# Kernel tuning notes

Hardware: AMD Instinct MI355X
Metric: run time of the kernel (lower is better)

The kernel has to match this reference:

```python
import jax, jax.numpy as jnp
from jax import lax
import numpy as np

K = 2000      # self.k: entries kept per sample
T_SC = 3      # number of IHT iterations
DN = ('NCHW', 'OIHW', 'NCHW')


def keep_k_largest(X, k):
    # Per-sample hard threshold: keep the k largest-magnitude entries of the
    # flattened [C,H,W] activations, zero the rest (exactly k kept, as in argsort).
    B = X.shape[0]
    flat = X.reshape(B, -1)                                # [B, N]
    _, idx = lax.top_k(jnp.abs(flat), k)                   # [B, k]
    vals = jnp.take_along_axis(flat, idx, axis=1)          # [B, k]
    out = jnp.zeros_like(flat).at[jnp.arange(B)[:, None], idx].set(vals)
    return out.reshape(X.shape)


def _D_apply(X, W_D):
    # ConvTranspose2d(numb_atom -> dp_channels), stride 1, no padding:
    # full correlation with the spatially flipped, io-swapped kernel.
    kh, kw = W_D.shape[2], W_D.shape[3]
    Wt = jnp.flip(jnp.transpose(W_D, (1, 0, 2, 3)), (2, 3))  # [dp, atoms, kh, kw]
    return lax.conv_general_dilated(X, Wt, (1, 1),
                                    [(kh - 1, kh - 1), (kw - 1, kw - 1)],
                                    dimension_numbers=DN)


def _Dt_apply(Z, W_D):
    # Conv2d(dp_channels -> numb_atom) VALID; D_trans.weight = D.weight.permute(0,1,3,2)
    Wt = jnp.transpose(W_D, (0, 1, 3, 2))                  # [atoms, dp, kh, kw]
    return lax.conv_general_dilated(Z, Wt, (1, 1), 'VALID', dimension_numbers=DN)


def setup_inputs() -> dict:
    key = jax.random.key(0)
    k1, k2, k3 = jax.random.split(key, 3)
    Y = jax.random.normal(k1, (32, 3, 64, 64), jnp.float32)
    X0 = jax.random.normal(k2, (32, 128, 57, 57), jnp.float32)   # random init X in forward
    W_D = jax.random.normal(k3, (128, 3, 8, 8), jnp.float32) * 0.05
    return {"Y": Y, "X0": X0, "W_D": W_D}


def reference(Y, X0, W_D):
    # HT_arg = X - D_trans(D(X) - Y); then T_SC hard-threshold iterations.
    HT_arg = X0 - _Dt_apply(_D_apply(X0, W_D) - Y, W_D)
    X = HT_arg
    for i in range(T_SC):
        X = keep_k_largest(HT_arg, K)
        if i < T_SC - 1:  # final HT_arg update in the original is unused
            HT_arg = X - _Dt_apply(_D_apply(X, W_D) - Y, W_D)
    return X
```

## Files before the change

kernel.cpp:

```cpp
#include <hip/hip_runtime.h>

#define BATCH 32
#define ATOMS 128
#define CCH 3
#define XH 57
#define XW 57
#define OHH 64
#define OWW 64
#define KSEL 2000
#define PIX (XH*XW)
#define NPS (ATOMS*PIX)
#define NTOT (BATCH*NPS)
#define RPS (CCH*OHH*OWW)
#define RTOT (BATCH*RPS)
#define CANDCAP 32768
#define NW 24576
#define WSEG 102
#define ZWORDS (32*2048 + 32*1024)

__global__ __launch_bounds__(256) void prep_k(const float* __restrict__ Wg,
    double* __restrict__ WDd, double* __restrict__ Wt2d,
    const float* __restrict__ Y, double* __restrict__ Rd,
    unsigned* __restrict__ zbuf) {
  int e = blockIdx.x * 256 + threadIdx.x;
  if (e < NW) {
    {
      int kw = e & 7; int t = e >> 3; int c = t % 3; t /= 3; int kh = t & 7; int a = t >> 3;
      WDd[e] = (double)Wg[(a*3 + c)*64 + kh*8 + kw];
    }
    {
      int a = e & 127; int t = e >> 7; int j = t & 7; int i = (t >> 3) & 7; int c = t >> 6;
      Wt2d[e] = (double)Wg[(a*3 + c)*64 + j*8 + i];
    }
  }
  if (e < RTOT) Rd[e] = -(double)Y[e];
  if (e < ZWORDS + 64) zbuf[e] = 0;
}

__global__ __launch_bounds__(256) void convD_k(const float* __restrict__ X,
    const double* __restrict__ WDd, double* __restrict__ Rd) {
  __shared__ double Xs[4][11][72];
  int p = blockIdx.x;
  int lg = (p & 7) * 256 + (p >> 3);
  int b = lg >> 6; int rem = lg & 63;
  int band = rem >> 2, quarter = rem & 3;
  int row0 = band * 4;
  int a_base = quarter * 32;
  int tid = threadIdx.x;
  int ox = tid & 63;
  int wv = __builtin_amdgcn_readfirstlane(tid >> 6);
  const float* Xb = X + (size_t)b * NPS;

  double acc[4][3];
#pragma unroll
  for (int ty = 0; ty < 4; ++ty)
#pragma unroll
    for (int c = 0; c < 3; ++c) acc[ty][c] = 0.0;

  for (int ch = 0; ch < 8; ++ch) {
    __syncthreads();
    for (int e = tid; e < 4 * 11 * 72; e += 256) {
      int ai = e / 792; int rem2 = e - ai * 792;
      int r = rem2 / 72; int ss = rem2 - r * 72;
      int gy = row0 - 7 + r;
      int xcol = ss - 7;
      int a = a_base + ch * 4 + ai;
      float v = 0.0f;
      if ((unsigned)xcol < (unsigned)XW && (unsigned)gy < (unsigned)XH)
        v = Xb[a * PIX + gy * XW + xcol];
      Xs[ai][r][ss] = (double)v;
    }
    __syncthreads();
    {
      int a = a_base + ch * 4 + wv;
      const double* Wa = WDd + a * 192;
#pragma unroll
      for (int r = 0; r < 11; ++r) {
        int gy = row0 - 7 + r;
        if ((unsigned)gy >= (unsigned)XH) continue;
        double xd[8];
#pragma unroll
        for (int t = 0; t < 8; ++t) xd[t] = Xs[wv][r][ox + t];
#pragma unroll
        for (int ty = 0; ty < 4; ++ty) {
          int kh = ty + 7 - r;
          if ((unsigned)kh < 8u) {
            const double* Wk = Wa + kh * 24;
#pragma unroll
            for (int kw = 0; kw < 8; ++kw) {
              acc[ty][0] = fma(xd[7 - kw], Wk[kw],      acc[ty][0]);
              acc[ty][1] = fma(xd[7 - kw], Wk[8 + kw],  acc[ty][1]);
              acc[ty][2] = fma(xd[7 - kw], Wk[16 + kw], acc[ty][2]);
            }
          }
        }
      }
    }
  }
#pragma unroll
  for (int ty = 0; ty < 4; ++ty) {
    int oy = row0 + ty;
#pragma unroll
    for (int c = 0; c < 3; ++c)
      atomicAdd(&Rd[((size_t)(b * CCH + c) << 12) + (oy << 6) + ox], acc[ty][c]);
  }
}

__global__ __launch_bounds__(256) void convD_sparse_k(const float* __restrict__ Wg,
    const int* __restrict__ nzidx, const float* __restrict__ nzval,
    const float* __restrict__ Y, float* __restrict__ R) {
  __shared__ double accd[512];
  __shared__ float Wf[8192];
  __shared__ int   li[KSEL];
  __shared__ float lv[KSEL];
  int p = blockIdx.x;
  int lg = (p & 7) * 96 + (p >> 3);
  int s = lg / 24; int r = lg % 24; int c = r >> 3; int band = r & 7;
  int row0 = band * 8;
  int tid = threadIdx.x;
  for (int e = tid; e < 512; e += 256) accd[e] = 0.0;
  for (int e = tid; e < 8192; e += 256) {
    int a = e >> 6, k2 = e & 63;
    Wf[e] = Wg[(a * 3 + c) * 64 + k2];
  }
  for (int e = tid; e < KSEL; e += 256) {
    li[e] = nzidx[s * KSEL + e];
    lv[e] = nzval[s * KSEL + e];
  }
  __syncthreads();
  int slot = tid >> 3, kw = tid & 7;
  for (int e = slot; e < KSEL; e += 32) {
    int idx = li[e];
    int a = (int)((unsigned)idx / 3249u);
    int pp = idx - a * 3249;
    int y = (int)((unsigned)pp / 57u);
    int x = pp - y * 57;
    int dy = y - row0;
    if (dy < -7 || dy > 7) continue;
    double val = (double)lv[e];
    const float* wp = Wf + (a << 6) + kw;
#pragma unroll
    for (int kh = 0; kh < 8; ++kh) {
      int rr = dy + kh;
      if ((unsigned)rr < 8u)
        __hip_atomic_fetch_add(&accd[(rr << 6) + x + kw],
                               val * (double)wp[kh << 3],
                               __ATOMIC_RELAXED, __HIP_MEMORY_SCOPE_WORKGROUP);
    }
  }
  __syncthreads();
  const float* Yb = Y + (((size_t)(s * CCH + c)) << 12) + (row0 << 6);
  float* Rb = R + (((size_t)(s * CCH + c)) << 12) + (row0 << 6);
  for (int e = tid; e < 512; e += 256)
    Rb[e] = (float)(accd[e] - (double)Yb[e]);
}

template <typename TR>
__global__ __launch_bounds__(256) void convDt_k(const TR* __restrict__ R,
    const double* __restrict__ Wt2d, const float* __restrict__ Xprev,
    float* __restrict__ HT, unsigned* __restrict__ g1) {
  __shared__ float Rl[3][15][72];
  __shared__ unsigned hh[1024];
  int p = blockIdx.x;
  int lg = (p & 7) * 512 + (p >> 3);
  int b = lg >> 7; int rem = lg & 127; int ag = rem >> 3; int by = rem & 7;
  int row0 = by * 8;
  int a0 = ag * 8;
  int tid = threadIdx.x;
  for (int e = tid; e < 1024; e += 256) hh[e] = 0;
  for (int e = tid; e < 3 * 15 * 72; e += 256) {
    int c = e / (15 * 72); int r2 = e - c * (15 * 72);
    int rr = r2 / 72; int cc = r2 - rr * 72;
    int gr = row0 + rr;
    float v = 0.0f;
    if (cc < OWW && gr < OHH)
      v = (float)R[((size_t)(b * CCH + c) << 12) + (gr << 6) + cc];
    Rl[c][rr][cc] = v;
  }
  __syncthreads();
  int x = tid & 63, yg = tid >> 6;
  int yb = yg * 2;
  double acc[8][2];
#pragma unroll
  for (int aa = 0; aa < 8; ++aa) { acc[aa][0] = 0.0; acc[aa][1] = 0.0; }

#pragma unroll 1
  for (int c = 0; c < 3; ++c) {
#pragma unroll 1
    for (int j = 0; j < 8; ++j) {
      double rw[9];
#pragma unroll
      for (int r = 0; r < 9; ++r) rw[r] = (double)Rl[c][yb + r][x + j];
#pragma unroll
      for (int i = 0; i < 8; ++i) {
        const double* wp = Wt2d + ((c * 8 + i) * 8 + j) * 128 + a0;
#pragma unroll
        for (int aa = 0; aa < 8; ++aa) {
          double w = wp[aa];
          acc[aa][0] = fma(rw[i + 0], w, acc[aa][0]);
          acc[aa][1] = fma(rw[i + 1], w, acc[aa][1]);
        }
      }
    }
  }
  if (x < XW) {
#pragma unroll
    for (int ty = 0; ty < 2; ++ty) {
      int yy = row0 + yb + ty;
      if (yy < XH) {
#pragma unroll
        for (int aa = 0; aa < 8; ++aa) {
          size_t xo = (size_t)(b * ATOMS + a0 + aa) * PIX + yy * XW + x;
          float fv = (float)((double)Xprev[xo] - acc[aa][ty]);
          HT[xo] = fv;
          unsigned u = __float_as_uint(fv) & 0x7fffffffu;
          unsigned bin = u >> 20;
          atomicAdd(&hh[bin >> 1], 1u << ((bin & 1) << 4));
        }
      }
    }
  }
  __syncthreads();
  unsigned* gp = g1 + (size_t)b * 2048;
  for (int e = tid; e < 1024; e += 256) {
    unsigned v = hh[e];
    unsigned lo = v & 0xffffu, hi = v >> 16;
    if (lo) atomicAdd(&gp[2 * e], lo);
    if (hi) atomicAdd(&gp[2 * e + 1], hi);
  }
}

__global__ __launch_bounds__(256) void hist2_k(const float* __restrict__ HT,
    const unsigned* __restrict__ g1, unsigned* __restrict__ g2,
    int* __restrict__ cand, int* __restrict__ candcnt) {
  __shared__ unsigned h[1024];
  __shared__ unsigned part[256];
  __shared__ int lidx[4096];
  __shared__ int lcnt, lbase, b1_sh;
  int tid = threadIdx.x;
  int s = blockIdx.x >> 5;
  int chunk = blockIdx.x & 31;
  const unsigned* hg1 = g1 + (size_t)s * 2048;
  unsigned psum = 0;
#pragma unroll
  for (int e = 0; e < 8; ++e) psum += hg1[tid * 8 + e];
  part[tid] = psum;
  for (int e = tid; e < 1024; e += 256) h[e] = 0;
  if (tid == 0) lcnt = 0;
  __syncthreads();
  if (tid == 0) {
    int Kv = KSEL;
    unsigned cumBefore = 0;
    int bsel = 0;
    for (int q = 255; q >= 0; --q) {
      unsigned ps = part[q];
      if ((int)(cumBefore + ps) >= Kv) {
        for (int e = q * 8 + 7;; --e) {
          unsigned c2 = cumBefore + hg1[e];
          if ((int)c2 >= Kv) { bsel = e; break; }
          cumBefore = c2;
        }
        break;
      }
      cumBefore += ps;
    }
    b1_sh = bsel;
  }
  __syncthreads();
  unsigned pre = (unsigned)b1_sh;
  const uint4* U4 = (const uint4*)(HT + (size_t)s * NPS);
  for (int i4 = chunk * 256 + tid; i4 < NPS / 4; i4 += 32 * 256) {
    uint4 v = U4[i4];
    unsigned uu[4] = {v.x, v.y, v.z, v.w};
#pragma unroll
    for (int t = 0; t < 4; ++t) {
      unsigned u = uu[t] & 0x7fffffffu;
      if ((u >> 20) == pre) {
        atomicAdd(&h[(u >> 10) & 1023], 1u);
        int pos = atomicAdd(&lcnt, 1);
        if (pos < 4096) lidx[pos] = i4 * 4 + t;
      }
    }
  }
  __syncthreads();
  if (tid == 0) {
    int n = lcnt < 4096 ? lcnt : 4096;
    lbase = atomicAdd(&candcnt[s], n);
  }
  __syncthreads();
  int n = lcnt < 4096 ? lcnt : 4096;
  int base = lbase;
  for (int e = tid; e < n; e += 256) {
    int g = base + e;
    if (g < CANDCAP) cand[s * CANDCAP + g] = lidx[e];
  }
  for (int e = tid; e < 1024; e += 256)
    if (h[e]) atomicAdd(&g2[s * 1024 + e], h[e]);
}

__global__ __launch_bounds__(256) void pass3_k(const float* __restrict__ HT,
    const int* __restrict__ cand, int* __restrict__ candcnt,
    const unsigned* __restrict__ g1, const unsigned* __restrict__ g2,
    int* __restrict__ nzcnt, unsigned* __restrict__ tau_out,
    int* __restrict__ cutoff_out) {
  int s = blockIdx.x;
  __shared__ unsigned h[1024];
  __shared__ unsigned part[256];
  __shared__ int eqidx[1024];
  __shared__ int eqn;
  __shared__ unsigned tau_sh;
  __shared__ int k3_sh;
  __shared__ int b1_sh, k1_sh, b2_sh, k2_sh;
  int t = threadIdx.x;
  const unsigned* hg1 = g1 + (size_t)s * 2048;
  unsigned s1 = 0;
#pragma unroll
  for (int e = 0; e < 8; ++e) s1 += hg1[t * 8 + e];
  part[t] = s1;
  for (int e = t; e < 1024; e += 256) h[e] = 0;
  if (t == 0) eqn = 0;
  __syncthreads();
  if (t == 0) {
    int Kv = KSEL;
    unsigned cumBefore = 0;
    int bsel = 0;
    for (int q = 255; q >= 0; --q) {
      unsigned ps = part[q];
      if ((int)(cumBefore + ps) >= Kv) {
        for (int e = q * 8 + 7;; --e) {
          unsigned c2 = cumBefore + hg1[e];
          if ((int)c2 >= Kv) { bsel = e; break; }
          cumBefore = c2;
        }
        break;
      }
      cumBefore += ps;
    }
    b1_sh = bsel;
    k1_sh = Kv - (int)cumBefore;
  }
  __syncthreads();
  const unsigned* hg = g2 + s * 1024;
  unsigned s2 = 0;
#pragma unroll
  for (int e = 0; e < 4; ++e) s2 += hg[t * 4 + e];
  part[t] = s2;
  __syncthreads();
  if (t == 0) {
    int Kv = k1_sh;
    unsigned cumBefore = 0;
    int bsel = 0;
    for (int q = 255; q >= 0; --q) {
      unsigned ps = part[q];
      if ((int)(cumBefore + ps) >= Kv) {
        for (int e = q * 4 + 3;; --e) {
          unsigned c2 = cumBefore + hg[e];
          if ((int)c2 >= Kv) { bsel = e; break; }
          cumBefore = c2;
        }
        break;
      }
      cumBefore += ps;
    }
    b2_sh = bsel;
    k2_sh = Kv - (int)cumBefore;
  }
  __syncthreads();
  int n = candcnt[s];
  if (n > CANDCAP) n = CANDCAP;
  unsigned pre21 = (((unsigned)b1_sh) << 10) | (unsigned)b2_sh;
  const unsigned* U = (const unsigned*)(HT + (size_t)s * NPS);
  for (int e = t; e < n; e += 256) {
    int i = cand[s * CANDCAP + e];
    unsigned u = U[i] & 0x7fffffffu;
    if ((u >> 10) == pre21) atomicAdd(&h[u & 1023], 1u);
  }
  __syncthreads();
  if (t == 0) {
    int Kv = k2_sh;
    unsigned cumBefore = 0;
    int b3 = 0;
    for (int e = 1023; e >= 0; --e) {
      unsigned c2 = cumBefore + h[e];
      if ((int)c2 >= Kv) { b3 = e; break; }
      cumBefore = c2;
    }
    tau_sh = (pre21 << 10) | (unsigned)b3;
    k3_sh = Kv - (int)cumBefore;
  }
  __syncthreads();
  unsigned tau = tau_sh;
  for (int e = t; e < n; e += 256) {
    int i = cand[s * CANDCAP + e];
    unsigned u = U[i] & 0x7fffffffu;
    if (u == tau) {
      int pos = atomicAdd(&eqn, 1);
      if (pos < 1024) eqidx[pos] = i;
    }
  }
  __syncthreads();
  if (t == 0) {
    int m = eqn < 1024 ? eqn : 1024;
    int k3 = k3_sh;
    int cutoff;
    if (k3 >= m) {
      cutoff = 0x7fffffff;
    } else {
      int last = -1;
      for (int r = 0; r < k3; ++r) {
        int mn = 0x7fffffff;
        for (int q = 0; q < m; ++q) {
          int v = eqidx[q];
          if (v > last && v < mn) mn = v;
        }
        last = mn;
      }
      cutoff = last;
    }
    tau_out[s] = tau;
    cutoff_out[s] = cutoff;
    candcnt[s] = 0;
    nzcnt[s] = 0;
  }
}

__global__ __launch_bounds__(256) void write_k(const float* __restrict__ HT,
    const unsigned* __restrict__ tau, const int* __restrict__ cutoff,
    float* __restrict__ Xo, int* __restrict__ nzidx, float* __restrict__ nzval,
    int* __restrict__ nzcnt, unsigned* __restrict__ zbuf) {
  __shared__ int lidx[2048];
  __shared__ float lval[2048];
  __shared__ int lcnt, lbase;
  int s = blockIdx.x / WSEG;
  int seg = blockIdx.x % WSEG;
  int tid = threadIdx.x;
  bool emit = (nzidx != nullptr);
  if (zbuf) {
    int e = blockIdx.x * 256 + tid;
    if (e < ZWORDS) zbuf[e] = 0;
  }
  if (tid == 0) lcnt = 0;
  __syncthreads();
  unsigned tt = tau[s];
  int co = cutoff[s];
  size_t sbase = (size_t)s * NPS;
  const float4* H4 = (const float4*)(HT + sbase);
  float4* X4 = (float4*)(Xo + sbase);
  int f0 = seg * 1024;
#pragma unroll
  for (int rr = 0; rr < 4; ++rr) {
    int i4 = f0 + rr * 256 + tid;
    if (i4 < NPS / 4) {
      float4 v = H4[i4];
      float vv[4] = {v.x, v.y, v.z, v.w};
      float oo[4];
#pragma unroll
      for (int t = 0; t < 4; ++t) {
        int il = i4 * 4 + t;
        unsigned u = __float_as_uint(vv[t]) & 0x7fffffffu;
        bool keep = (u > tt) || (u == tt && il <= co);
        oo[t] = keep ? vv[t] : 0.0f;
        if (keep && emit) {
          int pos = atomicAdd(&lcnt, 1);
          if (pos < 2048) { lidx[pos] = il; lval[pos] = vv[t]; }
        }
      }
      X4[i4] = make_float4(oo[0], oo[1], oo[2], oo[3]);
    }
  }
  if (!emit) return;
  __syncthreads();
  if (tid == 0) lbase = atomicAdd(&nzcnt[s], lcnt);
  __syncthreads();
  int n = lcnt < 2048 ? lcnt : 2048;
  int base = lbase;
  for (int e = tid; e < n; e += 256) {
    int g = base + e;
    if (g < KSEL) { nzidx[s * KSEL + g] = lidx[e]; nzval[s * KSEL + g] = lval[e]; }
  }
}

extern "C" void kernel_launch(void* const* d_in, const int* in_sizes, int n_in,
                              void* d_out, int out_size, void* d_ws, size_t ws_size,
                              hipStream_t stream) {
  const float* Y  = (const float*)d_in[0];
  const float* X0 = (const float*)d_in[1];
  const float* Wg = (const float*)d_in[2];
  float* Xout = (float*)d_out;

  double* WDd  = (double*)d_ws;
  double* Wt2d = WDd + NW;
  float* HT   = (float*)(Wt2d + NW);
  float* Rbuf = HT + NTOT;
  double* Rd  = (double*)(Rbuf + RTOT);
  unsigned* g1 = (unsigned*)(Rd + RTOT);
  unsigned* g2 = g1 + 32 * 2048;
  int* candcnt = (int*)(g2 + 32 * 1024);
  int* nzcnt = candcnt + 32;
  unsigned* tau = (unsigned*)(nzcnt + 32);
  int* cutoff = (int*)(tau + 32);
  int* cand = cutoff + 32;
  int* nzidx = cand + 32 * CANDCAP;
  float* nzval = (float*)(nzidx + 32 * KSEL);

  prep_k<<<dim3((RTOT + 255) / 256), dim3(256), 0, stream>>>(Wg, WDd, Wt2d, Y, Rd, g1);

  for (int it = 0; it < 3; ++it) {
    const float* Xsrc = (it == 0) ? X0 : (const float*)Xout;
    if (it == 0) {
      convD_k<<<dim3(2048), dim3(256), 0, stream>>>(Xsrc, WDd, Rd);
      convDt_k<double><<<dim3(4096), dim3(256), 0, stream>>>(Rd, Wt2d, Xsrc, HT, g1);
    } else {
      convD_sparse_k<<<dim3(BATCH * CCH * 8), dim3(256), 0, stream>>>(
          Wg, nzidx, nzval, Y, Rbuf);
      convDt_k<float><<<dim3(4096), dim3(256), 0, stream>>>(Rbuf, Wt2d, Xsrc, HT, g1);
    }
    hist2_k<<<dim3(BATCH * 32), dim3(256), 0, stream>>>(HT, g1, g2, cand, candcnt);
    pass3_k<<<dim3(BATCH), dim3(256), 0, stream>>>(HT, cand, candcnt, g1, g2,
                                                   nzcnt, tau, cutoff);
    bool last = (it == 2);
    write_k<<<dim3(BATCH * WSEG), dim3(256), 0, stream>>>(HT, tau, cutoff, Xout,
        last ? nullptr : nzidx, last ? nullptr : nzval, nzcnt,
        last ? nullptr : g1);
  }
}
```

Measured before the change: 1.020 ms.

## Fuse threshold write into histogram pass, resolve boundary bin in pass3

Removes the separate write_k pass. The second histogram kernel now writes the output directly: entries above the boundary bin are kept, entries below are zeroed, and boundary-bin entries are provisionally written. pass3 then rewrites only the candidate entries using the exact tau and cutoff, and also zeroes the g1/g2 histograms. This saves one full read of HT and one kernel launch per iteration, at the cost of more shared memory in histwrite_k (lower occupancy) and a serial scatter of candidates inside the 32-block pass3.

Result: faster. 944.0 us (-7.4%).

```diff
diff --git a/kernel.cpp b/kernel.cpp
--- a/kernel.cpp
+++ b/kernel.cpp
@@ -15,7 +15,6 @@
 #define RTOT (BATCH*RPS)
 #define CANDCAP 32768
 #define NW 24576
-#define WSEG 102
 #define ZWORDS (32*2048 + 32*1024)
 
 __global__ __launch_bounds__(256) void prep_k(const float* __restrict__ Wg,
@@ -230,13 +229,17 @@
   }
 }
 
-__global__ __launch_bounds__(256) void hist2_k(const float* __restrict__ HT,
+__global__ __launch_bounds__(256) void histwrite_k(const float* __restrict__ HT,
     const unsigned* __restrict__ g1, unsigned* __restrict__ g2,
-    int* __restrict__ cand, int* __restrict__ candcnt) {
+    int* __restrict__ cand, int* __restrict__ candcnt,
+    float* __restrict__ Xo, int* __restrict__ nzidx, float* __restrict__ nzval,
+    int* __restrict__ nzcnt, int emit) {
   __shared__ unsigned h[1024];
   __shared__ unsigned part[256];
   __shared__ int lidx[4096];
-  __shared__ int lcnt, lbase, b1_sh;
+  __shared__ int kidx[2048];
+  __shared__ float kval[2048];
+  __shared__ int lcnt, lbase, kcnt, kbase, b1_sh;
   int tid = threadIdx.x;
   int s = blockIdx.x >> 5;
   int chunk = blockIdx.x & 31;
@@ -246,7 +249,7 @@
   for (int e = 0; e < 8; ++e) psum += hg1[tid * 8 + e];
   part[tid] = psum;
   for (int e = tid; e < 1024; e += 256) h[e] = 0;
-  if (tid == 0) lcnt = 0;
+  if (tid == 0) { lcnt = 0; kcnt = 0; }
   __syncthreads();
   if (tid == 0) {
     int Kv = KSEL;
@@ -268,31 +271,57 @@
   }
   __syncthreads();
   unsigned pre = (unsigned)b1_sh;
-  const uint4* U4 = (const uint4*)(HT + (size_t)s * NPS);
+  size_t sbase = (size_t)s * NPS;
+  const uint4* U4 = (const uint4*)(HT + sbase);
+  float4* X4 = (float4*)(Xo + sbase);
   for (int i4 = chunk * 256 + tid; i4 < NPS / 4; i4 += 32 * 256) {
     uint4 v = U4[i4];
     unsigned uu[4] = {v.x, v.y, v.z, v.w};
+    float oo[4];
 #pragma unroll
     for (int t = 0; t < 4; ++t) {
+      int il = i4 * 4 + t;
       unsigned u = uu[t] & 0x7fffffffu;
-      if ((u >> 20) == pre) {
+      unsigned bin = u >> 20;
+      float val = __uint_as_float(uu[t]);
+      if (bin > pre) {
+        oo[t] = val;
+        if (emit) {
+          int pos = atomicAdd(&kcnt, 1);
+          if (pos < 2048) { kidx[pos] = il; kval[pos] = val; }
+        }
+      } else if (bin < pre) {
+        oo[t] = 0.0f;
+      } else {
+        oo[t] = val;
         atomicAdd(&h[(u >> 10) & 1023], 1u);
         int pos = atomicAdd(&lcnt, 1);
-        if (pos < 4096) lidx[pos] = i4 * 4 + t;
-      }
-    }
+        if (pos < 4096) lidx[pos] = il;
+      }
+    }
+    X4[i4] = make_float4(oo[0], oo[1], oo[2], oo[3]);
   }
   __syncthreads();
   if (tid == 0) {
     int n = lcnt < 4096 ? lcnt : 4096;
     lbase = atomicAdd(&candcnt[s], n);
+    if (emit) {
+      int kn = kcnt < 2048 ? kcnt : 2048;
+      kbase = atomicAdd(&nzcnt[s], kn);
+    }
   }
   __syncthreads();
   int n = lcnt < 4096 ? lcnt : 4096;
-  int base = lbase;
   for (int e = tid; e < n; e += 256) {
-    int g = base + e;
+    int g = lbase + e;
     if (g < CANDCAP) cand[s * CANDCAP + g] = lidx[e];
+  }
+  if (emit) {
+    int kn = kcnt < 2048 ? kcnt : 2048;
+    for (int e = tid; e < kn; e += 256) {
+      int g = kbase + e;
+      if (g < KSEL) { nzidx[s * KSEL + g] = kidx[e]; nzval[s * KSEL + g] = kval[e]; }
+    }
   }
   for (int e = tid; e < 1024; e += 256)
     if (h[e]) atomicAdd(&g2[s * 1024 + e], h[e]);
@@ -300,25 +329,27 @@
 
 __global__ __launch_bounds__(256) void pass3_k(const float* __restrict__ HT,
     const int* __restrict__ cand, int* __restrict__ candcnt,
-    const unsigned* __restrict__ g1, const unsigned* __restrict__ g2,
-    int* __restrict__ nzcnt, unsigned* __restrict__ tau_out,
-    int* __restrict__ cutoff_out) {
+    unsigned* __restrict__ g1, unsigned* __restrict__ g2,
+    float* __restrict__ Xo, int* __restrict__ nzidx, float* __restrict__ nzval,
+    int* __restrict__ nzcnt, int emit) {
   int s = blockIdx.x;
   __shared__ unsigned h[1024];
   __shared__ unsigned part[256];
   __shared__ int eqidx[1024];
-  __shared__ int eqn;
+  __shared__ int kidx[2048];
+  __shared__ float kval[2048];
+  __shared__ int eqn, kcnt, kbase;
   __shared__ unsigned tau_sh;
-  __shared__ int k3_sh;
+  __shared__ int k3_sh, cutoff_sh;
   __shared__ int b1_sh, k1_sh, b2_sh, k2_sh;
   int t = threadIdx.x;
-  const unsigned* hg1 = g1 + (size_t)s * 2048;
+  unsigned* hg1 = g1 + (size_t)s * 2048;
   unsigned s1 = 0;
 #pragma unroll
   for (int e = 0; e < 8; ++e) s1 += hg1[t * 8 + e];
   part[t] = s1;
   for (int e = t; e < 1024; e += 256) h[e] = 0;
-  if (t == 0) eqn = 0;
+  if (t == 0) { eqn = 0; kcnt = 0; }
   __syncthreads();
   if (t == 0) {
     int Kv = KSEL;
@@ -340,7 +371,7 @@
     k1_sh = Kv - (int)cumBefore;
   }
   __syncthreads();
-  const unsigned* hg = g2 + s * 1024;
+  unsigned* hg = g2 + s * 1024;
   unsigned s2 = 0;
 #pragma unroll
   for (int e = 0; e < 4; ++e) s2 += hg[t * 4 + e];
@@ -417,67 +448,40 @@
       }
       cutoff = last;
     }
-    tau_out[s] = tau;
-    cutoff_out[s] = cutoff;
-    candcnt[s] = 0;
-    nzcnt[s] = 0;
-  }
-}
-
-__global__ __launch_bounds__(256) void write_k(const float* __restrict__ HT,
-    const unsigned* __restrict__ tau, const int* __restrict__ cutoff,
-    float* __restrict__ Xo, int* __restrict__ nzidx, float* __restrict__ nzval,
-    int* __restrict__ nzcnt, unsigned* __restrict__ zbuf) {
-  __shared__ int lidx[2048];
-  __shared__ float lval[2048];
-  __shared__ int lcnt, lbase;
-  int s = blockIdx.x / WSEG;
-  int seg = blockIdx.x % WSEG;
-  int tid = threadIdx.x;
-  bool emit = (nzidx != nullptr);
-  if (zbuf) {
-    int e = blockIdx.x * 256 + tid;
-    if (e < ZWORDS) zbuf[e] = 0;
-  }
-  if (tid == 0) lcnt = 0;
-  __syncthreads();
-  unsigned tt = tau[s];
-  int co = cutoff[s];
-  size_t sbase = (size_t)s * NPS;
-  const float4* H4 = (const float4*)(HT + sbase);
-  float4* X4 = (float4*)(Xo + sbase);
-  int f0 = seg * 1024;
-#pragma unroll
-  for (int rr = 0; rr < 4; ++rr) {
-    int i4 = f0 + rr * 256 + tid;
-    if (i4 < NPS / 4) {
-      float4 v = H4[i4];
-      float vv[4] = {v.x, v.y, v.z, v.w};
-      float oo[4];
-#pragma unroll
-      for (int t = 0; t < 4; ++t) {
-        int il = i4 * 4 + t;
-        unsigned u = __float_as_uint(vv[t]) & 0x7fffffffu;
-        bool keep = (u > tt) || (u == tt && il <= co);
-        oo[t] = keep ? vv[t] : 0.0f;
-        if (keep && emit) {
-          int pos = atomicAdd(&lcnt, 1);
-          if (pos < 2048) { lidx[pos] = il; lval[pos] = vv[t]; }
-        }
-      }
-      X4[i4] = make_float4(oo[0], oo[1], oo[2], oo[3]);
-    }
-  }
-  if (!emit) return;
-  __syncthreads();
-  if (tid == 0) lbase = atomicAdd(&nzcnt[s], lcnt);
-  __syncthreads();
-  int n = lcnt < 2048 ? lcnt : 2048;
-  int base = lbase;
-  for (int e = tid; e < n; e += 256) {
-    int g = base + e;
-    if (g < KSEL) { nzidx[s * KSEL + g] = lidx[e]; nzval[s * KSEL + g] = lval[e]; }
-  }
+    cutoff_sh = cutoff;
+  }
+  __syncthreads();
+  int co = cutoff_sh;
+  float* Xs = Xo + (size_t)s * NPS;
+  for (int e = t; e < n; e += 256) {
+    int i = cand[s * CANDCAP + e];
+    unsigned uval = U[i];
+    unsigned u = uval & 0x7fffffffu;
+    bool keep = (u > tau) || (u == tau && i <= co);
+    float val = __uint_as_float(uval);
+    Xs[i] = keep ? val : 0.0f;
+    if (keep && emit) {
+      int pos = atomicAdd(&kcnt, 1);
+      if (pos < 2048) { kidx[pos] = i; kval[pos] = val; }
+    }
+  }
+  __syncthreads();
+  if (emit) {
+    if (t == 0) {
+      int kn = kcnt < 2048 ? kcnt : 2048;
+      kbase = atomicAdd(&nzcnt[s], kn);
+    }
+    __syncthreads();
+    int kn = kcnt < 2048 ? kcnt : 2048;
+    for (int e = t; e < kn; e += 256) {
+      int g = kbase + e;
+      if (g < KSEL) { nzidx[s * KSEL + g] = kidx[e]; nzval[s * KSEL + g] = kval[e]; }
+    }
+  }
+  __syncthreads();
+  for (int e = t; e < 2048; e += 256) hg1[e] = 0;
+  for (int e = t; e < 1024; e += 256) hg[e] = 0;
+  if (t == 0) { candcnt[s] = 0; nzcnt[s] = 0; }
 }
 
 extern "C" void kernel_launch(void* const* d_in, const int* in_sizes, int n_in,
@@ -497,9 +501,7 @@
   unsigned* g2 = g1 + 32 * 2048;
   int* candcnt = (int*)(g2 + 32 * 1024);
   int* nzcnt = candcnt + 32;
-  unsigned* tau = (unsigned*)(nzcnt + 32);
-  int* cutoff = (int*)(tau + 32);
-  int* cand = cutoff + 32;
+  int* cand = nzcnt + 32;
   int* nzidx = cand + 32 * CANDCAP;
   float* nzval = (float*)(nzidx + 32 * KSEL);
 
@@ -515,12 +517,10 @@
           Wg, nzidx, nzval, Y, Rbuf);
       convDt_k<float><<<dim3(4096), dim3(256), 0, stream>>>(Rbuf, Wt2d, Xsrc, HT, g1);
     }
-    hist2_k<<<dim3(BATCH * 32), dim3(256), 0, stream>>>(HT, g1, g2, cand, candcnt);
-    pass3_k<<<dim3(BATCH), dim3(256), 0, stream>>>(HT, cand, candcnt, g1, g2,
-                                                   nzcnt, tau, cutoff);
-    bool last = (it == 2);
-    write_k<<<dim3(BATCH * WSEG), dim3(256), 0, stream>>>(HT, tau, cutoff, Xout,
-        last ? nullptr : nzidx, last ? nullptr : nzval, nzcnt,
-        last ? nullptr : g1);
-  }
-}
+    int emit = (it < 2) ? 1 : 0;
+    histwrite_k<<<dim3(BATCH * 32), dim3(256), 0, stream>>>(
+        HT, g1, g2, cand, candcnt, Xout, nzidx, nzval, nzcnt, emit);
+    pass3_k<<<dim3(BATCH), dim3(256), 0, stream>>>(
+        HT, cand, candcnt, g1, g2, Xout, nzidx, nzval, nzcnt, emit);
+  }
+}
```
